# Performance work log

Hardware: AMD Instinct MI355X
Metric: run time of the kernel (lower is better)

The kernel has to match this reference:

```python
import jax, jax.numpy as jnp
import numpy as np

N_HEADS = 16
QUANT_BITS = 8


def fake_quantize(x, bits=QUANT_BITS):
    # Global max-abs fake quantization with STE (grad = identity).
    if bits >= 16:
        return x
    max_val = jnp.max(jnp.abs(x))
    half_levels = jnp.asarray(2.0 ** (bits - 1), x.dtype)
    q = jnp.round(x / max_val * half_levels) / half_levels * max_val
    q = jnp.where(max_val > 0, q, x)
    return x + jax.lax.stop_gradient(q - x)


def qat_linear(x, W, b):
    # torch nn.Linear: y = x @ W.T + b, with fake-quant on input and output.
    xq = fake_quantize(x)
    y = jnp.einsum('bsd,od->bso', xq, W) + b
    return fake_quantize(y)


def setup_inputs() -> dict:
    key = jax.random.key(0)
    ks = jax.random.split(key, 9)
    d = 1024
    B, S = 2, 2048
    scale = 1.0 / np.sqrt(d)
    return {
        'x': jax.random.normal(ks[0], (B, S, d), jnp.float32),
        'Wq': jax.random.normal(ks[1], (d, d), jnp.float32) * scale,
        'bq': jax.random.normal(ks[2], (d,), jnp.float32) * 0.01,
        'Wk': jax.random.normal(ks[3], (d, d), jnp.float32) * scale,
        'bk': jax.random.normal(ks[4], (d,), jnp.float32) * 0.01,
        'Wv': jax.random.normal(ks[5], (d, d), jnp.float32) * scale,
        'bv': jax.random.normal(ks[6], (d,), jnp.float32) * 0.01,
        'Wo': jax.random.normal(ks[7], (d, d), jnp.float32) * scale,
        'bo': jax.random.normal(ks[8], (d,), jnp.float32) * 0.01,
    }


def reference(x, Wq, bq, Wk, bk, Wv, bv, Wo, bo):
    B, S, d_model = x.shape
    d_k = d_model // N_HEADS

    def split_heads(t):  # [B,S,D] -> [B,H,S,dk]
        return t.reshape(B, S, N_HEADS, d_k).transpose(0, 2, 1, 3)

    Q = split_heads(qat_linear(x, Wq, bq))
    K = split_heads(qat_linear(x, Wk, bk))
    V = split_heads(qat_linear(x, Wv, bv))

    scores = jnp.einsum('bhqd,bhkd->bhqk', Q, K) / jnp.sqrt(jnp.asarray(d_k, x.dtype))
    attn = jax.nn.softmax(scores, axis=-1)  # dropout = identity (deterministic ref)
    out = jnp.einsum('bhqk,bhkd->bhqd', attn, V)
    out = out.transpose(0, 2, 1, 3).reshape(B, S, d_model)
    return qat_linear(out, Wo, bo)
```

## Files before the change

kernel.cpp:

```cpp
#include <hip/hip_runtime.h>
#include <math.h>

#define DMODEL 1024
#define SEQ    2048
#define NELEM  4194304
#define N4     (NELEM / 4)

typedef __attribute__((ext_vector_type(8))) short short8;
typedef __attribute__((ext_vector_type(4))) short short4v;
typedef __attribute__((ext_vector_type(4))) float f32x4;

#if __has_builtin(__builtin_amdgcn_exp2f)
#define EXP2(x) __builtin_amdgcn_exp2f(x)
#else
#define EXP2(x) exp2f(x)
#endif

__device__ __forceinline__ void gl2lds16(const unsigned short* g, unsigned short* l) {
    __builtin_amdgcn_global_load_lds(
        (const __attribute__((address_space(1))) unsigned int*)g,
        (__attribute__((address_space(3))) unsigned int*)l,
        16, 0, 0);
}

__device__ __forceinline__ float fq(float x, float m) {
    float t = x / m * 128.0f;
    float r = rintf(t);
    float q = r * 0.0078125f * m;
    return (m > 0.0f) ? q : x;
}
__device__ __forceinline__ unsigned short f2bf(float f) {
    unsigned int u = __float_as_uint(f);
    u += 0x7FFFu + ((u >> 16) & 1u);
    return (unsigned short)(u >> 16);
}
__device__ __forceinline__ float bf2f(unsigned short h) {
    return __uint_as_float(((unsigned int)h) << 16);
}
__device__ __forceinline__ unsigned short qint(float x, float m) {
    float i = rintf(x / m * 128.0f);
    return (unsigned short)(__float_as_uint(i) >> 16);
}

__device__ __forceinline__ void block_max_atomic(float v, float* red, unsigned int* slot) {
    const int t = threadIdx.x;
    red[t] = v;
    __syncthreads();
    #pragma unroll
    for (int s = 128; s > 0; s >>= 1) {
        if (t < s) red[t] = fmaxf(red[t], red[t + s]);
        __syncthreads();
    }
    if (t == 0) atomicMax(slot, __float_as_uint(red[0]));
}

__global__ __launch_bounds__(256) void absmax_kernel(const float* __restrict__ x, int n4,
                                                     unsigned int* __restrict__ slot) {
    __shared__ float red[256];
    float m = 0.0f;
    const float4* x4 = (const float4*)x;
    for (int i = blockIdx.x * 256 + threadIdx.x; i < n4; i += gridDim.x * 256) {
        float4 v = x4[i];
        m = fmaxf(m, fmaxf(fmaxf(fabsf(v.x), fabsf(v.y)), fmaxf(fabsf(v.z), fabsf(v.w))));
    }
    block_max_atomic(m, red, slot);
}

__global__ __launch_bounds__(256) void quant_int_kernel(const float* __restrict__ src,
                                                        unsigned short* __restrict__ dst,
                                                        const unsigned int* __restrict__ slot,
                                                        int n4) {
    const float m = __uint_as_float(*slot);
    const float4* s4 = (const float4*)src;
    for (int i = blockIdx.x * 256 + threadIdx.x; i < n4; i += gridDim.x * 256) {
        float4 v = s4[i];
        ushort4 o;
        o.x = qint(v.x, m); o.y = qint(v.y, m); o.z = qint(v.z, m); o.w = qint(v.w, m);
        ((ushort4*)dst)[i] = o;
    }
}

__global__ __launch_bounds__(256) void quant_out_kernel(float* __restrict__ Y,
                                                        const unsigned int* __restrict__ slot,
                                                        int n4) {
    const float m = __uint_as_float(*slot);
    float4* y4 = (float4*)Y;
    for (int i = blockIdx.x * 256 + threadIdx.x; i < n4; i += gridDim.x * 256) {
        float4 v = y4[i];
        v.x = fq(v.x, m); v.y = fq(v.y, m); v.z = fq(v.z, m); v.w = fq(v.w, m);
        y4[i] = v;
    }
}

__global__ __launch_bounds__(256) void wsplit_kernel(
    const float* __restrict__ W0, const float* __restrict__ W1,
    const float* __restrict__ W2, const float* __restrict__ W3,
    unsigned short* __restrict__ H0, unsigned short* __restrict__ L0,
    unsigned short* __restrict__ H1, unsigned short* __restrict__ L1,
    unsigned short* __restrict__ H2, unsigned short* __restrict__ L2,
    unsigned short* __restrict__ H3, unsigned short* __restrict__ L3) {
    const int z = blockIdx.y;
    const float* W = (z == 0) ? W0 : (z == 1) ? W1 : (z == 2) ? W2 : W3;
    unsigned short* H = (z == 0) ? H0 : (z == 1) ? H1 : (z == 2) ? H2 : H3;
    unsigned short* L = (z == 0) ? L0 : (z == 1) ? L1 : (z == 2) ? L2 : L3;
    const int i = blockIdx.x * 256 + threadIdx.x;
    float4 w = ((const float4*)W)[i];
    ushort4 h, l;
    h.x = f2bf(w.x); l.x = f2bf(w.x - bf2f(h.x));
    h.y = f2bf(w.y); l.y = f2bf(w.y - bf2f(h.y));
    h.z = f2bf(w.z); l.z = f2bf(w.z - bf2f(h.z));
    h.w = f2bf(w.w); l.w = f2bf(w.w - bf2f(h.w));
    ((ushort4*)H)[i] = h;
    ((ushort4*)L)[i] = l;
}

__global__ __launch_bounds__(256) void vtrans_quant(const float* __restrict__ Vraw,
                                                    unsigned short* __restrict__ Vti,
                                                    const unsigned int* __restrict__ slot) {
    __shared__ float tile[64][65];
    const float mv = __uint_as_float(*slot);
    const int t = threadIdx.x;
    const int s0 = blockIdx.x << 6;
    const int bh = blockIdx.y;
    const int b = bh >> 4, h = bh & 15;
    const int rr = t >> 4;
    const int cc = (t & 15) << 2;
    #pragma unroll
    for (int rep = 0; rep < 4; rep++) {
        int srow = rep * 16 + rr;
        float4 v = *(const float4*)&Vraw[(size_t)b * SEQ * DMODEL + (size_t)(s0 + srow) * DMODEL + h * 64 + cc];
        tile[srow][cc + 0] = v.x; tile[srow][cc + 1] = v.y;
        tile[srow][cc + 2] = v.z; tile[srow][cc + 3] = v.w;
    }
    __syncthreads();
    #pragma unroll
    for (int rep = 0; rep < 4; rep++) {
        int drow = rep * 16 + rr;
        ushort4 o;
        o.x = qint(tile[cc + 0][drow], mv);
        o.y = qint(tile[cc + 1][drow], mv);
        o.z = qint(tile[cc + 2][drow], mv);
        o.w = qint(tile[cc + 3][drow], mv);
        *(ushort4*)&Vti[(size_t)bh * 64 * SEQ + (size_t)drow * SEQ + s0 + cc] = o;
    }
}

template<int BN>
__global__ __launch_bounds__(256) void gemm_mfma(
    const unsigned short* __restrict__ Ai, const unsigned int* __restrict__ mSlot,
    const unsigned short* __restrict__ Wh0, const unsigned short* __restrict__ Wl0,
    const float* __restrict__ b0, float* __restrict__ O0, unsigned int* __restrict__ s0,
    const unsigned short* __restrict__ Wh1, const unsigned short* __restrict__ Wl1,
    const float* __restrict__ b1, float* __restrict__ O1, unsigned int* __restrict__ s1,
    const unsigned short* __restrict__ Wh2, const unsigned short* __restrict__ Wl2,
    const float* __restrict__ b2, float* __restrict__ O2, unsigned int* __restrict__ s2) {
    constexpr int NI = BN / 32;
    __shared__ __align__(16) unsigned short As[128 * 32];
    __shared__ __align__(16) unsigned short Bh[BN * 32];
    __shared__ __align__(16) unsigned short Bl[BN * 32];
    __shared__ float red[256];

    const int z = blockIdx.z;
    const unsigned short* Wh = (z == 0) ? Wh0 : (z == 1) ? Wh1 : Wh2;
    const unsigned short* Wl = (z == 0) ? Wl0 : (z == 1) ? Wl1 : Wl2;
    const float* bias = (z == 0) ? b0 : (z == 1) ? b1 : b2;
    float* O = (z == 0) ? O0 : (z == 1) ? O1 : O2;
    unsigned int* slotOut = (z == 0) ? s0 : (z == 1) ? s1 : s2;

    const float mA = __uint_as_float(*mSlot);
    const int t = threadIdx.x;
    const int lane = t & 63, w = t >> 6;
    const int ml = lane & 15, qd = lane >> 4;
    const int wm = w & 1, wn = w >> 1;
    const int m0 = blockIdx.y << 7;
    const int n0 = blockIdx.x * BN;

    const int lr = lane >> 2;
    const int lc = (lane & 3) << 3;
    const unsigned short* Asrc = Ai + (size_t)(m0 + w * 32 + lr) * DMODEL + lc;
    const unsigned short* Hsrc = Wh + (size_t)(n0 + w * (BN / 4) + lr) * DMODEL + lc;
    const unsigned short* Lsrc = Wl + (size_t)(n0 + w * (BN / 4) + lr) * DMODEL + lc;
    unsigned short* Adst = &As[(w * 32) * 32];
    unsigned short* Hdst = &Bh[(w * (BN / 4)) * 32];
    unsigned short* Ldst = &Bl[(w * (BN / 4)) * 32];

    f32x4 acc[4][NI];
    #pragma unroll
    for (int mi = 0; mi < 4; mi++)
        #pragma unroll
        for (int ni = 0; ni < NI; ni++) acc[mi][ni] = (f32x4){0.f, 0.f, 0.f, 0.f};

    for (int k0 = 0; k0 < DMODEL; k0 += 32) {
        __syncthreads();
        gl2lds16(Asrc + k0,               Adst);
        gl2lds16(Asrc + k0 + 16 * DMODEL, Adst + 16 * 32);
        if constexpr (BN == 128) {
            gl2lds16(Hsrc + k0,               Hdst);
            gl2lds16(Hsrc + k0 + 16 * DMODEL, Hdst + 16 * 32);
            gl2lds16(Lsrc + k0,               Ldst);
            gl2lds16(Lsrc + k0 + 16 * DMODEL, Ldst + 16 * 32);
        } else {
            gl2lds16(Hsrc + k0, Hdst);
            gl2lds16(Lsrc + k0, Ldst);
        }
        __syncthreads();

        short8 af[4];
        #pragma unroll
        for (int mi = 0; mi < 4; mi++)
            af[mi] = *(const short8*)&As[(wm * 64 + mi * 16 + ml) * 32 + qd * 8];
        #pragma unroll
        for (int ni = 0; ni < NI; ni++) {
            short8 bh = *(const short8*)&Bh[(wn * (BN / 2) + ni * 16 + ml) * 32 + qd * 8];
            short8 bl = *(const short8*)&Bl[(wn * (BN / 2) + ni * 16 + ml) * 32 + qd * 8];
            #pragma unroll
            for (int mi = 0; mi < 4; mi++) {
                acc[mi][ni] = __builtin_amdgcn_mfma_f32_16x16x32_bf16(af[mi], bh, acc[mi][ni], 0, 0, 0);
                acc[mi][ni] = __builtin_amdgcn_mfma_f32_16x16x32_bf16(af[mi], bl, acc[mi][ni], 0, 0, 0);
            }
        }
    }

    const float s = mA * 0.0078125f;
    float lmax = 0.0f;
    #pragma unroll
    for (int ni = 0; ni < NI; ni++) {
        const int col = n0 + wn * (BN / 2) + ni * 16 + ml;
        const float bc = bias[col];
        #pragma unroll
        for (int mi = 0; mi < 4; mi++) {
            #pragma unroll
            for (int r = 0; r < 4; r++) {
                int row = m0 + wm * 64 + mi * 16 + qd * 4 + r;
                float v = acc[mi][ni][r] * s + bc;
                lmax = fmaxf(lmax, fabsf(v));
                O[row * DMODEL + col] = v;
            }
        }
    }
    block_max_atomic(lmax, red, slotOut);
}

__global__ __launch_bounds__(256) void attn_mfma(
    const float* __restrict__ Qraw, const unsigned short* __restrict__ Ki,
    const unsigned short* __restrict__ Vti, const unsigned int* __restrict__ slots,
    float* __restrict__ Out, unsigned int* __restrict__ moSlot) {
    __shared__ __align__(16) unsigned short Ks[2][64 * 72];
    __shared__ __align__(16) unsigned short Vt[2][64 * 72];
    __shared__ float red[256];
    union U8 { short8 v; unsigned short u[8]; };
    union U4 { short4v v; unsigned short u[4]; };

    const int t = threadIdx.x;
    const int lane = t & 63, w = t >> 6;
    const int ml = lane & 15, qd = lane >> 4;
    const int q0 = blockIdx.x << 6;
    const int bh = blockIdx.y;
    const int b = bh >> 4, h = bh & 15;
    const float mq = __uint_as_float(slots[1]);
    const float mk = __uint_as_float(slots[2]);
    const float mv = __uint_as_float(slots[3]);
    const float c2 = (mq * 0.0078125f) * (mk * 0.0078125f) * 0.125f * 1.4426950408889634f;
    const int baseQ = b * SEQ * DMODEL + h * 64;
    const int qg = q0 + w * 16 + ml;

    short8 bq[2];
    {
        const float* src = Qraw + baseQ + qg * DMODEL + qd * 8;
        #pragma unroll
        for (int c = 0; c < 2; c++) {
            float4 v0 = *(const float4*)(src + c * 32);
            float4 v1 = *(const float4*)(src + c * 32 + 4);
            U8 tmp;
            tmp.u[0] = qint(v0.x, mq); tmp.u[1] = qint(v0.y, mq);
            tmp.u[2] = qint(v0.z, mq); tmp.u[3] = qint(v0.w, mq);
            tmp.u[4] = qint(v1.x, mq); tmp.u[5] = qint(v1.y, mq);
            tmp.u[6] = qint(v1.z, mq); tmp.u[7] = qint(v1.w, mq);
            bq[c] = tmp.v;
        }
    }

    f32x4 oacc[4];
    #pragma unroll
    for (int i = 0; i < 4; i++) oacc[i] = (f32x4){0.f, 0.f, 0.f, 0.f};
    float mrun = -INFINITY, lrun = 0.0f;

    const int sr = t >> 2;
    const int sc = (t & 3) << 4;
    const unsigned short* kstage = Ki + baseQ + (size_t)sr * DMODEL + sc;
    const unsigned short* vstage = Vti + (size_t)bh * 64 * SEQ + (size_t)sr * SEQ + sc;

    {
        short8 a = *(const short8*)kstage;
        short8 bb = *(const short8*)(kstage + 8);
        short8 c = *(const short8*)vstage;
        short8 d = *(const short8*)(vstage + 8);
        *(short8*)&Ks[0][sr * 72 + sc] = a;
        *(short8*)&Ks[0][sr * 72 + sc + 8] = bb;
        *(short8*)&Vt[0][sr * 72 + sc] = c;
        *(short8*)&Vt[0][sr * 72 + sc + 8] = d;
    }
    __syncthreads();

    for (int it = 0; it < 32; it++) {
        const int cur = it & 1;
        short8 nk0, nk1, nv0, nv1;
        if (it < 31) {
            const size_t ko = (size_t)(it + 1) * 64;
            nk0 = *(const short8*)(kstage + ko * DMODEL);
            nk1 = *(const short8*)(kstage + ko * DMODEL + 8);
            nv0 = *(const short8*)(vstage + ko);
            nv1 = *(const short8*)(vstage + ko + 8);
        }

        f32x4 sacc[4];
        #pragma unroll
        for (int tau = 0; tau < 4; tau++) {
            short8 a0 = *(const short8*)&Ks[cur][(tau * 16 + ml) * 72 + qd * 8];
            short8 a1 = *(const short8*)&Ks[cur][(tau * 16 + ml) * 72 + 32 + qd * 8];
            f32x4 z4 = (f32x4){0.f, 0.f, 0.f, 0.f};
            z4 = __builtin_amdgcn_mfma_f32_16x16x32_bf16(a0, bq[0], z4, 0, 0, 0);
            sacc[tau] = __builtin_amdgcn_mfma_f32_16x16x32_bf16(a1, bq[1], z4, 0, 0, 0);
        }

        float tmax = fmaxf(fmaxf(fmaxf(sacc[0][0], sacc[0][1]), fmaxf(sacc[0][2], sacc[0][3])),
                           fmaxf(fmaxf(sacc[1][0], sacc[1][1]), fmaxf(sacc[1][2], sacc[1][3])));
        tmax = fmaxf(tmax, fmaxf(fmaxf(fmaxf(sacc[2][0], sacc[2][1]), fmaxf(sacc[2][2], sacc[2][3])),
                                 fmaxf(fmaxf(sacc[3][0], sacc[3][1]), fmaxf(sacc[3][2], sacc[3][3]))));
        tmax = fmaxf(tmax, __shfl_xor(tmax, 16));
        tmax = fmaxf(tmax, __shfl_xor(tmax, 32));
        const float mnew = fmaxf(mrun, tmax);
        const float alpha = EXP2((mrun - mnew) * c2);
        const float mc = mnew * c2;
        float p[4][4];
        float ls = 0.0f;
        #pragma unroll
        for (int tau = 0; tau < 4; tau++)
            #pragma unroll
            for (int r = 0; r < 4; r++) {
                float pv = EXP2(sacc[tau][r] * c2 - mc);
                p[tau][r] = pv;
                ls += pv;
            }
        ls += __shfl_xor(ls, 16);
        ls += __shfl_xor(ls, 32);
        lrun = lrun * alpha + ls;
        mrun = mnew;

        short4v phi[4], plo[4];
        #pragma unroll
        for (int tau = 0; tau < 4; tau++) {
            U4 hh, ll;
            #pragma unroll
            for (int r = 0; r < 4; r++) {
                unsigned int u = __float_as_uint(p[tau][r]);
                unsigned int uh = (u + 0x8000u) & 0xFFFF0000u;
                hh.u[r] = (unsigned short)(uh >> 16);
                float lf = p[tau][r] - __uint_as_float(uh);
                ll.u[r] = (unsigned short)(__float_as_uint(lf) >> 16);
            }
            phi[tau] = hh.v;
            plo[tau] = ll.v;
        }

        #pragma unroll
        for (int i = 0; i < 4; i++) {
            oacc[i][0] *= alpha; oacc[i][1] *= alpha;
            oacc[i][2] *= alpha; oacc[i][3] *= alpha;
        }

        #pragma unroll
        for (int td = 0; td < 4; td++) {
            #pragma unroll
            for (int tau = 0; tau < 4; tau++) {
                short4v av = *(const short4v*)&Vt[cur][(td * 16 + ml) * 72 + tau * 16 + qd * 4];
                oacc[td] = __builtin_amdgcn_mfma_f32_16x16x16bf16_1k(av, phi[tau], oacc[td], 0, 0, 0);
                oacc[td] = __builtin_amdgcn_mfma_f32_16x16x16bf16_1k(av, plo[tau], oacc[td], 0, 0, 0);
            }
        }

        if (it < 31) {
            *(short8*)&Ks[cur ^ 1][sr * 72 + sc] = nk0;
            *(short8*)&Ks[cur ^ 1][sr * 72 + sc + 8] = nk1;
            *(short8*)&Vt[cur ^ 1][sr * 72 + sc] = nv0;
            *(short8*)&Vt[cur ^ 1][sr * 72 + sc + 8] = nv1;
        }
        __syncthreads();
    }

    const float inv = (mv * 0.0078125f) / lrun;
    float lmax = 0.0f;
    #pragma unroll
    for (int td = 0; td < 4; td++) {
        float4 o;
        o.x = oacc[td][0] * inv;
        o.y = oacc[td][1] * inv;
        o.z = oacc[td][2] * inv;
        o.w = oacc[td][3] * inv;
        lmax = fmaxf(lmax, fmaxf(fmaxf(fabsf(o.x), fabsf(o.y)), fmaxf(fabsf(o.z), fabsf(o.w))));
        *(float4*)&Out[baseQ + (size_t)qg * DMODEL + td * 16 + qd * 4] = o;
    }
    block_max_atomic(lmax, red, moSlot);
}

extern "C" void kernel_launch(void* const* d_in, const int* in_sizes, int n_in,
                              void* d_out, int out_size, void* d_ws, size_t ws_size,
                              hipStream_t stream) {
    const float* x  = (const float*)d_in[0];
    const float* Wq = (const float*)d_in[1];
    const float* bq = (const float*)d_in[2];
    const float* Wk = (const float*)d_in[3];
    const float* bk = (const float*)d_in[4];
    const float* Wv = (const float*)d_in[5];
    const float* bv = (const float*)d_in[6];
    const float* Wo = (const float*)d_in[7];
    const float* bo = (const float*)d_in[8];
    float* out = (float*)d_out;

    const size_t MB = 1024 * 1024;
    unsigned int* slots = (unsigned int*)d_ws;
    char* p = (char*)d_ws + 256;
    unsigned short* WqH = (unsigned short*)(p + 0 * MB);
    unsigned short* WqL = (unsigned short*)(p + 2 * MB);
    unsigned short* WkH = (unsigned short*)(p + 4 * MB);
    unsigned short* WkL = (unsigned short*)(p + 6 * MB);
    unsigned short* WvH = (unsigned short*)(p + 8 * MB);
    unsigned short* WvL = (unsigned short*)(p + 10 * MB);
    unsigned short* WoH = (unsigned short*)(p + 12 * MB);
    unsigned short* WoL = (unsigned short*)(p + 14 * MB);
    unsigned short* Xi  = (unsigned short*)(p + 16 * MB);
    float* RA  = (float*)(p + 24 * MB);
    float* RB  = (float*)(p + 40 * MB);
    unsigned short* Vti = (unsigned short*)(p + 56 * MB);
    unsigned short* Ki  = (unsigned short*)(p + 4 * MB);
    unsigned short* Oi  = (unsigned short*)RA;
    float* Qraw = out;

    hipMemsetAsync(d_ws, 0, 256, stream);

    wsplit_kernel<<<dim3(1024, 4), 256, 0, stream>>>(Wq, Wk, Wv, Wo,
        WqH, WqL, WkH, WkL, WvH, WvL, WoH, WoL);
    absmax_kernel<<<1024, 256, 0, stream>>>(x, N4, slots + 0);
    quant_int_kernel<<<1024, 256, 0, stream>>>(x, Xi, slots + 0, N4);

    gemm_mfma<128><<<dim3(8, 32, 3), 256, 0, stream>>>(Xi, slots + 0,
        WqH, WqL, bq, Qraw, slots + 1,
        WkH, WkL, bk, RA,   slots + 2,
        WvH, WvL, bv, RB,   slots + 3);
    quant_int_kernel<<<1024, 256, 0, stream>>>(RA, Ki, slots + 2, N4);
    vtrans_quant<<<dim3(32, 32), 256, 0, stream>>>(RB, Vti, slots + 3);

    attn_mfma<<<dim3(32, 32), 256, 0, stream>>>(Qraw, Ki, Vti, slots, RB, slots + 4);
    quant_int_kernel<<<1024, 256, 0, stream>>>(RB, Oi, slots + 4, N4);

    gemm_mfma<64><<<dim3(16, 32, 1), 256, 0, stream>>>(Oi, slots + 4,
        WoH, WoL, bo, out, slots + 5,
        WoH, WoL, bo, out, slots + 5,
        WoH, WoL, bo, out, slots + 5);
    quant_out_kernel<<<1024, 256, 0, stream>>>(out, slots + 5, N4);
}
```

Before: 331.2 us.

## Double queries per attention block, merge small kernels, shrink QKV GEMM tile

The attention kernel now gives each warp two 16-row query groups (128 queries per block), so every K/V tile staged in LDS feeds twice as many MFMAs and K/V global traffic per query is halved. The weight split and input absmax are merged into one launch, as are the K quantization and the V transpose-quantize. The QKV GEMM moves from a 128 tile to a 64 tile to launch more blocks. In exchange, the attention kernel uses more registers and runs half as many blocks (512), which may lower occupancy.

```diff
diff --git a/kernel.cpp b/kernel.cpp
--- a/kernel.cpp
+++ b/kernel.cpp
@@ -54,52 +54,26 @@
     if (t == 0) atomicMax(slot, __float_as_uint(red[0]));
 }
 
-__global__ __launch_bounds__(256) void absmax_kernel(const float* __restrict__ x, int n4,
-                                                     unsigned int* __restrict__ slot) {
-    __shared__ float red[256];
-    float m = 0.0f;
-    const float4* x4 = (const float4*)x;
-    for (int i = blockIdx.x * 256 + threadIdx.x; i < n4; i += gridDim.x * 256) {
-        float4 v = x4[i];
-        m = fmaxf(m, fmaxf(fmaxf(fabsf(v.x), fabsf(v.y)), fmaxf(fabsf(v.z), fabsf(v.w))));
-    }
-    block_max_atomic(m, red, slot);
-}
-
-__global__ __launch_bounds__(256) void quant_int_kernel(const float* __restrict__ src,
-                                                        unsigned short* __restrict__ dst,
-                                                        const unsigned int* __restrict__ slot,
-                                                        int n4) {
-    const float m = __uint_as_float(*slot);
-    const float4* s4 = (const float4*)src;
-    for (int i = blockIdx.x * 256 + threadIdx.x; i < n4; i += gridDim.x * 256) {
-        float4 v = s4[i];
-        ushort4 o;
-        o.x = qint(v.x, m); o.y = qint(v.y, m); o.z = qint(v.z, m); o.w = qint(v.w, m);
-        ((ushort4*)dst)[i] = o;
-    }
-}
-
-__global__ __launch_bounds__(256) void quant_out_kernel(float* __restrict__ Y,
-                                                        const unsigned int* __restrict__ slot,
-                                                        int n4) {
-    const float m = __uint_as_float(*slot);
-    float4* y4 = (float4*)Y;
-    for (int i = blockIdx.x * 256 + threadIdx.x; i < n4; i += gridDim.x * 256) {
-        float4 v = y4[i];
-        v.x = fq(v.x, m); v.y = fq(v.y, m); v.z = fq(v.z, m); v.w = fq(v.w, m);
-        y4[i] = v;
-    }
-}
-
-__global__ __launch_bounds__(256) void wsplit_kernel(
+__global__ __launch_bounds__(256) void wsplit_absmax(
     const float* __restrict__ W0, const float* __restrict__ W1,
     const float* __restrict__ W2, const float* __restrict__ W3,
     unsigned short* __restrict__ H0, unsigned short* __restrict__ L0,
     unsigned short* __restrict__ H1, unsigned short* __restrict__ L1,
     unsigned short* __restrict__ H2, unsigned short* __restrict__ L2,
-    unsigned short* __restrict__ H3, unsigned short* __restrict__ L3) {
+    unsigned short* __restrict__ H3, unsigned short* __restrict__ L3,
+    const float* __restrict__ x, int n4, unsigned int* __restrict__ slot) {
+    __shared__ float red[256];
     const int z = blockIdx.y;
+    if (z == 4) {
+        float m = 0.0f;
+        const float4* x4 = (const float4*)x;
+        for (int i = blockIdx.x * 256 + threadIdx.x; i < n4; i += gridDim.x * 256) {
+            float4 v = x4[i];
+            m = fmaxf(m, fmaxf(fmaxf(fabsf(v.x), fabsf(v.y)), fmaxf(fabsf(v.z), fabsf(v.w))));
+        }
+        block_max_atomic(m, red, slot);
+        return;
+    }
     const float* W = (z == 0) ? W0 : (z == 1) ? W1 : (z == 2) ? W2 : W3;
     unsigned short* H = (z == 0) ? H0 : (z == 1) ? H1 : (z == 2) ? H2 : H3;
     unsigned short* L = (z == 0) ? L0 : (z == 1) ? L1 : (z == 2) ? L2 : L3;
@@ -114,14 +88,53 @@
     ((ushort4*)L)[i] = l;
 }
 
-__global__ __launch_bounds__(256) void vtrans_quant(const float* __restrict__ Vraw,
-                                                    unsigned short* __restrict__ Vti,
-                                                    const unsigned int* __restrict__ slot) {
+__global__ __launch_bounds__(256) void quant_int_kernel(const float* __restrict__ src,
+                                                        unsigned short* __restrict__ dst,
+                                                        const unsigned int* __restrict__ slot,
+                                                        int n4) {
+    const float m = __uint_as_float(*slot);
+    const float4* s4 = (const float4*)src;
+    for (int i = blockIdx.x * 256 + threadIdx.x; i < n4; i += gridDim.x * 256) {
+        float4 v = s4[i];
+        ushort4 o;
+        o.x = qint(v.x, m); o.y = qint(v.y, m); o.z = qint(v.z, m); o.w = qint(v.w, m);
+        ((ushort4*)dst)[i] = o;
+    }
+}
+
+__global__ __launch_bounds__(256) void quant_out_kernel(float* __restrict__ Y,
+                                                        const unsigned int* __restrict__ slot,
+                                                        int n4) {
+    const float m = __uint_as_float(*slot);
+    float4* y4 = (float4*)Y;
+    for (int i = blockIdx.x * 256 + threadIdx.x; i < n4; i += gridDim.x * 256) {
+        float4 v = y4[i];
+        v.x = fq(v.x, m); v.y = fq(v.y, m); v.z = fq(v.z, m); v.w = fq(v.w, m);
+        y4[i] = v;
+    }
+}
+
+__global__ __launch_bounds__(256) void quantK_vtrans(
+    const float* __restrict__ Kraw, unsigned short* __restrict__ Ki,
+    const unsigned int* __restrict__ slotK,
+    const float* __restrict__ Vraw, unsigned short* __restrict__ Vti,
+    const unsigned int* __restrict__ slotV, int n4) {
     __shared__ float tile[64][65];
-    const float mv = __uint_as_float(*slot);
+    if (blockIdx.y == 0) {
+        const float m = __uint_as_float(*slotK);
+        const float4* s4 = (const float4*)Kraw;
+        for (int i = blockIdx.x * 256 + threadIdx.x; i < n4; i += gridDim.x * 256) {
+            float4 v = s4[i];
+            ushort4 o;
+            o.x = qint(v.x, m); o.y = qint(v.y, m); o.z = qint(v.z, m); o.w = qint(v.w, m);
+            ((ushort4*)Ki)[i] = o;
+        }
+        return;
+    }
+    const float mv = __uint_as_float(*slotV);
     const int t = threadIdx.x;
-    const int s0 = blockIdx.x << 6;
-    const int bh = blockIdx.y;
+    const int s0 = (blockIdx.x & 31) << 6;
+    const int bh = blockIdx.x >> 5;
     const int b = bh >> 4, h = bh & 15;
     const int rr = t >> 4;
     const int cc = (t & 15) << 2;
@@ -254,7 +267,7 @@
     const int t = threadIdx.x;
     const int lane = t & 63, w = t >> 6;
     const int ml = lane & 15, qd = lane >> 4;
-    const int q0 = blockIdx.x << 6;
+    const int q0 = blockIdx.x << 7;
     const int bh = blockIdx.y;
     const int b = bh >> 4, h = bh & 15;
     const float mq = __uint_as_float(slots[1]);
@@ -262,11 +275,13 @@
     const float mv = __uint_as_float(slots[3]);
     const float c2 = (mq * 0.0078125f) * (mk * 0.0078125f) * 0.125f * 1.4426950408889634f;
     const int baseQ = b * SEQ * DMODEL + h * 64;
-    const int qg = q0 + w * 16 + ml;
-
-    short8 bq[2];
-    {
-        const float* src = Qraw + baseQ + qg * DMODEL + qd * 8;
+    const int qgA = q0 + w * 32 + ml;
+    const int qgB = qgA + 16;
+
+    short8 bq[2][2];
+    #pragma unroll
+    for (int g = 0; g < 2; g++) {
+        const float* src = Qraw + baseQ + (size_t)(g ? qgB : qgA) * DMODEL + qd * 8;
         #pragma unroll
         for (int c = 0; c < 2; c++) {
             float4 v0 = *(const float4*)(src + c * 32);
@@ -276,14 +291,16 @@
             tmp.u[2] = qint(v0.z, mq); tmp.u[3] = qint(v0.w, mq);
             tmp.u[4] = qint(v1.x, mq); tmp.u[5] = qint(v1.y, mq);
             tmp.u[6] = qint(v1.z, mq); tmp.u[7] = qint(v1.w, mq);
-            bq[c] = tmp.v;
-        }
-    }
-
-    f32x4 oacc[4];
-    #pragma unroll
-    for (int i = 0; i < 4; i++) oacc[i] = (f32x4){0.f, 0.f, 0.f, 0.f};
-    float mrun = -INFINITY, lrun = 0.0f;
+            bq[g][c] = tmp.v;
+        }
+    }
+
+    f32x4 oacc[2][4];
+    #pragma unroll
+    for (int g = 0; g < 2; g++)
+        #pragma unroll
+        for (int i = 0; i < 4; i++) oacc[g][i] = (f32x4){0.f, 0.f, 0.f, 0.f};
+    float mrun[2] = {-INFINITY, -INFINITY}, lrun[2] = {0.f, 0.f};
 
     const int sr = t >> 2;
     const int sc = (t & 3) << 4;
@@ -313,69 +330,73 @@
             nv1 = *(const short8*)(vstage + ko + 8);
         }
 
-        f32x4 sacc[4];
+        f32x4 sacc[2][4];
         #pragma unroll
         for (int tau = 0; tau < 4; tau++) {
             short8 a0 = *(const short8*)&Ks[cur][(tau * 16 + ml) * 72 + qd * 8];
             short8 a1 = *(const short8*)&Ks[cur][(tau * 16 + ml) * 72 + 32 + qd * 8];
-            f32x4 z4 = (f32x4){0.f, 0.f, 0.f, 0.f};
-            z4 = __builtin_amdgcn_mfma_f32_16x16x32_bf16(a0, bq[0], z4, 0, 0, 0);
-            sacc[tau] = __builtin_amdgcn_mfma_f32_16x16x32_bf16(a1, bq[1], z4, 0, 0, 0);
-        }
-
-        float tmax = fmaxf(fmaxf(fmaxf(sacc[0][0], sacc[0][1]), fmaxf(sacc[0][2], sacc[0][3])),
-                           fmaxf(fmaxf(sacc[1][0], sacc[1][1]), fmaxf(sacc[1][2], sacc[1][3])));
-        tmax = fmaxf(tmax, fmaxf(fmaxf(fmaxf(sacc[2][0], sacc[2][1]), fmaxf(sacc[2][2], sacc[2][3])),
-                                 fmaxf(fmaxf(sacc[3][0], sacc[3][1]), fmaxf(sacc[3][2], sacc[3][3]))));
-        tmax = fmaxf(tmax, __shfl_xor(tmax, 16));
-        tmax = fmaxf(tmax, __shfl_xor(tmax, 32));
-        const float mnew = fmaxf(mrun, tmax);
-        const float alpha = EXP2((mrun - mnew) * c2);
-        const float mc = mnew * c2;
-        float p[4][4];
-        float ls = 0.0f;
-        #pragma unroll
-        for (int tau = 0; tau < 4; tau++)
-            #pragma unroll
-            for (int r = 0; r < 4; r++) {
-                float pv = EXP2(sacc[tau][r] * c2 - mc);
-                p[tau][r] = pv;
-                ls += pv;
-            }
-        ls += __shfl_xor(ls, 16);
-        ls += __shfl_xor(ls, 32);
-        lrun = lrun * alpha + ls;
-        mrun = mnew;
-
-        short4v phi[4], plo[4];
-        #pragma unroll
-        for (int tau = 0; tau < 4; tau++) {
-            U4 hh, ll;
-            #pragma unroll
-            for (int r = 0; r < 4; r++) {
-                unsigned int u = __float_as_uint(p[tau][r]);
-                unsigned int uh = (u + 0x8000u) & 0xFFFF0000u;
-                hh.u[r] = (unsigned short)(uh >> 16);
-                float lf = p[tau][r] - __uint_as_float(uh);
-                ll.u[r] = (unsigned short)(__float_as_uint(lf) >> 16);
-            }
-            phi[tau] = hh.v;
-            plo[tau] = ll.v;
-        }
-
-        #pragma unroll
-        for (int i = 0; i < 4; i++) {
-            oacc[i][0] *= alpha; oacc[i][1] *= alpha;
-            oacc[i][2] *= alpha; oacc[i][3] *= alpha;
-        }
+            #pragma unroll
+            for (int g = 0; g < 2; g++) {
+                f32x4 z4 = (f32x4){0.f, 0.f, 0.f, 0.f};
+                z4 = __builtin_amdgcn_mfma_f32_16x16x32_bf16(a0, bq[g][0], z4, 0, 0, 0);
+                sacc[g][tau] = __builtin_amdgcn_mfma_f32_16x16x32_bf16(a1, bq[g][1], z4, 0, 0, 0);
+            }
+        }
+
+        float alpha[2];
+        short4v phi[2][4], plo[2][4];
+        #pragma unroll
+        for (int g = 0; g < 2; g++) {
+            float tmax = fmaxf(fmaxf(fmaxf(sacc[g][0][0], sacc[g][0][1]), fmaxf(sacc[g][0][2], sacc[g][0][3])),
+                               fmaxf(fmaxf(sacc[g][1][0], sacc[g][1][1]), fmaxf(sacc[g][1][2], sacc[g][1][3])));
+            tmax = fmaxf(tmax, fmaxf(fmaxf(fmaxf(sacc[g][2][0], sacc[g][2][1]), fmaxf(sacc[g][2][2], sacc[g][2][3])),
+                                     fmaxf(fmaxf(sacc[g][3][0], sacc[g][3][1]), fmaxf(sacc[g][3][2], sacc[g][3][3]))));
+            tmax = fmaxf(tmax, __shfl_xor(tmax, 16));
+            tmax = fmaxf(tmax, __shfl_xor(tmax, 32));
+            const float mnew = fmaxf(mrun[g], tmax);
+            alpha[g] = EXP2((mrun[g] - mnew) * c2);
+            const float mc = mnew * c2;
+            float ls = 0.0f;
+            #pragma unroll
+            for (int tau = 0; tau < 4; tau++) {
+                U4 hh, ll;
+                #pragma unroll
+                for (int r = 0; r < 4; r++) {
+                    float pv = EXP2(sacc[g][tau][r] * c2 - mc);
+                    ls += pv;
+                    unsigned int u = __float_as_uint(pv);
+                    unsigned int uh = (u + 0x8000u) & 0xFFFF0000u;
+                    hh.u[r] = (unsigned short)(uh >> 16);
+                    float lf = pv - __uint_as_float(uh);
+                    ll.u[r] = (unsigned short)(__float_as_uint(lf) >> 16);
+                }
+                phi[g][tau] = hh.v;
+                plo[g][tau] = ll.v;
+            }
+            ls += __shfl_xor(ls, 16);
+            ls += __shfl_xor(ls, 32);
+            lrun[g] = lrun[g] * alpha[g] + ls;
+            mrun[g] = mnew;
+        }
+
+        #pragma unroll
+        for (int g = 0; g < 2; g++)
+            #pragma unroll
+            for (int i = 0; i < 4; i++) {
+                oacc[g][i][0] *= alpha[g]; oacc[g][i][1] *= alpha[g];
+                oacc[g][i][2] *= alpha[g]; oacc[g][i][3] *= alpha[g];
+            }
 
         #pragma unroll
         for (int td = 0; td < 4; td++) {
             #pragma unroll
             for (int tau = 0; tau < 4; tau++) {
                 short4v av = *(const short4v*)&Vt[cur][(td * 16 + ml) * 72 + tau * 16 + qd * 4];
-                oacc[td] = __builtin_amdgcn_mfma_f32_16x16x16bf16_1k(av, phi[tau], oacc[td], 0, 0, 0);
-                oacc[td] = __builtin_amdgcn_mfma_f32_16x16x16bf16_1k(av, plo[tau], oacc[td], 0, 0, 0);
+                #pragma unroll
+                for (int g = 0; g < 2; g++) {
+                    oacc[g][td] = __builtin_amdgcn_mfma_f32_16x16x16bf16_1k(av, phi[g][tau], oacc[g][td], 0, 0, 0);
+                    oacc[g][td] = __builtin_amdgcn_mfma_f32_16x16x16bf16_1k(av, plo[g][tau], oacc[g][td], 0, 0, 0);
+                }
             }
         }
 
@@ -388,17 +409,21 @@
         __syncthreads();
     }
 
-    const float inv = (mv * 0.0078125f) / lrun;
     float lmax = 0.0f;
     #pragma unroll
-    for (int td = 0; td < 4; td++) {
-        float4 o;
-        o.x = oacc[td][0] * inv;
-        o.y = oacc[td][1] * inv;
-        o.z = oacc[td][2] * inv;
-        o.w = oacc[td][3] * inv;
-        lmax = fmaxf(lmax, fmaxf(fmaxf(fabsf(o.x), fabsf(o.y)), fmaxf(fabsf(o.z), fabsf(o.w))));
-        *(float4*)&Out[baseQ + (size_t)qg * DMODEL + td * 16 + qd * 4] = o;
+    for (int g = 0; g < 2; g++) {
+        const float inv = (mv * 0.0078125f) / lrun[g];
+        const int qg = g ? qgB : qgA;
+        #pragma unroll
+        for (int td = 0; td < 4; td++) {
+            float4 o;
+            o.x = oacc[g][td][0] * inv;
+            o.y = oacc[g][td][1] * inv;
+            o.z = oacc[g][td][2] * inv;
+            o.w = oacc[g][td][3] * inv;
+            lmax = fmaxf(lmax, fmaxf(fmaxf(fabsf(o.x), fabsf(o.y)), fmaxf(fabsf(o.z), fabsf(o.w))));
+            *(float4*)&Out[baseQ + (size_t)qg * DMODEL + td * 16 + qd * 4] = o;
+        }
     }
     block_max_atomic(lmax, red, moSlot);
 }
@@ -438,19 +463,18 @@
 
     hipMemsetAsync(d_ws, 0, 256, stream);
 
-    wsplit_kernel<<<dim3(1024, 4), 256, 0, stream>>>(Wq, Wk, Wv, Wo,
-        WqH, WqL, WkH, WkL, WvH, WvL, WoH, WoL);
-    absmax_kernel<<<1024, 256, 0, stream>>>(x, N4, slots + 0);
+    wsplit_absmax<<<dim3(1024, 5), 256, 0, stream>>>(Wq, Wk, Wv, Wo,
+        WqH, WqL, WkH, WkL, WvH, WvL, WoH, WoL, x, N4, slots + 0);
     quant_int_kernel<<<1024, 256, 0, stream>>>(x, Xi, slots + 0, N4);
 
-    gemm_mfma<128><<<dim3(8, 32, 3), 256, 0, stream>>>(Xi, slots + 0,
+    gemm_mfma<64><<<dim3(16, 32, 3), 256, 0, stream>>>(Xi, slots + 0,
         WqH, WqL, bq, Qraw, slots + 1,
         WkH, WkL, bk, RA,   slots + 2,
         WvH, WvL, bv, RB,   slots + 3);
-    quant_int_kernel<<<1024, 256, 0, stream>>>(RA, Ki, slots + 2, N4);
-    vtrans_quant<<<dim3(32, 32), 256, 0, stream>>>(RB, Vti, slots + 3);
-
-    attn_mfma<<<dim3(32, 32), 256, 0, stream>>>(Qraw, Ki, Vti, slots, RB, slots + 4);
+    quantK_vtrans<<<dim3(1024, 2), 256, 0, stream>>>(RA, Ki, slots + 2,
+                                                     RB, Vti, slots + 3, N4);
+
+    attn_mfma<<<dim3(16, 32), 256, 0, stream>>>(Qraw, Ki, Vti, slots, RB, slots + 4);
     quant_int_kernel<<<1024, 256, 0, stream>>>(RB, Oi, slots + 4, N4);
 
     gemm_mfma<64><<<dim3(16, 32, 1), 256, 0, stream>>>(Oi, slots + 4,
```

Result: faster. 314.2 us (-5.1%).
